# Performance work log

Measured on AMD Instinct MI355X. Metric: run time of the kernel, lower is better.

The kernel has to match this reference:

```python
import math
import jax, jax.numpy as jnp
import numpy as np


def get_alibi_slopes(n_heads: int) -> jnp.ndarray:
    def _pow2_slopes(n):
        i = jnp.arange(1, n + 1, dtype=jnp.float32)
        return jnp.power(2.0, -8.0 * i / n)
    if n_heads & (n_heads - 1) == 0:
        return _pow2_slopes(n_heads)
    nearest = 2 ** math.ceil(math.log2(n_heads))
    full = _pow2_slopes(nearest)
    half = nearest // 2
    half_slopes = _pow2_slopes(half)
    extra = full[jnp.arange(half) * 2 + 1]
    return jnp.concatenate([half_slopes, extra])[:n_heads]


def build_alibi_bias(n_heads: int, T: int, causal: bool = True) -> jnp.ndarray:
    slopes = get_alibi_slopes(n_heads)  # (H,)
    idx = jnp.arange(T)
    rel = jnp.abs(idx[:, None] - idx[None, :]).astype(jnp.float32)  # (T,T)
    bias = -slopes[:, None, None] * rel[None]  # (H,T,T)
    if causal:
        future = idx[None, :] > idx[:, None]
        bias = jnp.where(future[None], -jnp.inf, bias)
    return bias


def setup_inputs() -> dict:
    key = jax.random.key(0)
    ks = jax.random.split(key, 5)
    B, T, C = 2, 2048, 1024
    s = 0.02
    return {
        "x": jax.random.normal(ks[0], (B, T, C), dtype=jnp.float32),
        "Wq": jax.random.normal(ks[1], (C, C), dtype=jnp.float32) * s,
        "Wk": jax.random.normal(ks[2], (C, C), dtype=jnp.float32) * s,
        "Wv": jax.random.normal(ks[3], (C, C), dtype=jnp.float32) * s,
        "Wo": jax.random.normal(ks[4], (C, C), dtype=jnp.float32) * s,
    }


def reference(x, Wq, Wk, Wv, Wo):
    B, T, C = x.shape
    H = 16
    D = C // H
    scale = D ** -0.5
    # torch nn.Linear(bias=False): y = x @ W.T
    def proj_split(W):
        t = jnp.einsum('btc,dc->btd', x, W)
        return t.reshape(B, T, H, D).transpose(0, 2, 1, 3)  # (B,H,T,D)
    q, k, v = proj_split(Wq), proj_split(Wk), proj_split(Wv)
    scores = jnp.einsum('bhtd,bhsd->bhts', q, k) * scale  # (B,H,T,T)
    bias = build_alibi_bias(H, T, causal=True)  # (H,T,T)
    scores = scores + bias[None]
    attn = jax.nn.softmax(scores, axis=-1)
    out = jnp.einsum('bhts,bhsd->bhtd', attn, v)
    out = out.transpose(0, 2, 1, 3).reshape(B, T, C)
    return jnp.einsum('btc,dc->btd', out, Wo)
```

## Files before the change

### kernel.cpp

```cpp
#include <hip/hip_runtime.h>
#include <hip/hip_bf16.h>


typedef _Float16 f16;
typedef f16 f16x2 __attribute__((ext_vector_type(2)));
typedef f16 f16x4 __attribute__((ext_vector_type(4)));
typedef f16 f16x8 __attribute__((ext_vector_type(8)));
typedef float f32x4 __attribute__((ext_vector_type(4)));
typedef float f32x16 __attribute__((ext_vector_type(16)));

#define LOG2E 1.4426950408889634f
#define LDK 40
#define LDA 72
#define LDV 136

__device__ __forceinline__ f16x4 pk4(f32x4 v) {
  f16x2 a = __builtin_bit_cast(f16x2, __builtin_amdgcn_cvt_pkrtz(v[0], v[1]));
  f16x2 b = __builtin_bit_cast(f16x2, __builtin_amdgcn_cvt_pkrtz(v[2], v[3]));
  f16x4 r; r[0] = a[0]; r[1] = a[1]; r[2] = b[0]; r[3] = b[1];
  return r;
}
__device__ __forceinline__ f16x8 mkp(const float* e, int p) {
  f16x2 a = __builtin_bit_cast(f16x2, __builtin_amdgcn_cvt_pkrtz(e[4*p+0], e[4*p+1]));
  f16x2 b = __builtin_bit_cast(f16x2, __builtin_amdgcn_cvt_pkrtz(e[4*p+2], e[4*p+3]));
  f16x2 c = __builtin_bit_cast(f16x2, __builtin_amdgcn_cvt_pkrtz(e[8+4*p+0], e[8+4*p+1]));
  f16x2 d = __builtin_bit_cast(f16x2, __builtin_amdgcn_cvt_pkrtz(e[8+4*p+2], e[8+4*p+3]));
  f16x8 r;
  r[0]=a[0]; r[1]=a[1]; r[2]=b[0]; r[3]=b[1];
  r[4]=c[0]; r[5]=c[1]; r[6]=d[0]; r[7]=d[1];
  return r;
}

__global__ __launch_bounds__(256) void cvt_f32_f16(
    const float* __restrict__ x, const float* __restrict__ wq,
    const float* __restrict__ wk, const float* __restrict__ wv,
    const float* __restrict__ wo,
    f16* __restrict__ dx, f16* __restrict__ dwq, f16* __restrict__ dwk,
    f16* __restrict__ dwv, f16* __restrict__ dwo) {
  const float* src; f16* dst; int n;
  switch (blockIdx.y) {
    case 0:  src = x;  dst = dx;  n = 4194304; break;
    case 1:  src = wq; dst = dwq; n = 1048576; break;
    case 2:  src = wk; dst = dwk; n = 1048576; break;
    case 3:  src = wv; dst = dwv; n = 1048576; break;
    default: src = wo; dst = dwo; n = 1048576; break;
  }
  int i = (blockIdx.x * 256 + (int)threadIdx.x) * 8;
  if (i >= n) return;
  f32x4 a = *(const f32x4*)(src + i);
  f32x4 b = *(const f32x4*)(src + i + 4);
  f16x8 o;
  f16x4 lo4 = pk4(a), hi4 = pk4(b);
#pragma unroll
  for (int j = 0; j < 4; j++) { o[j] = lo4[j]; o[j + 4] = hi4[j]; }
  *(f16x8*)(dst + i) = o;
}

__device__ __forceinline__ void gemm_core(const f16* __restrict__ A,
                                          const f16* __restrict__ W,
                                          int m0, int n0,
                                          f16* lA, f16* lW,
                                          f32x4 acc[4][4]) {
  const int tid = threadIdx.x;
  const int lane = tid & 63, w = tid >> 6;
  const int wm = w & 1, wn = w >> 1;
  const int q = lane & 15, quad = lane >> 4;
  const int r0 = tid >> 2, c0 = (tid & 3) * 8;

  const f16* Ap = A + (m0 + r0) * 1024 + c0;
  const f16* Wp = W + (n0 + r0) * 1024 + c0;
  f16x8 a0 = *(const f16x8*)(Ap);
  f16x8 a1 = *(const f16x8*)(Ap + 64 * 1024);
  f16x8 w0 = *(const f16x8*)(Wp);
  f16x8 w1 = *(const f16x8*)(Wp + 64 * 1024);

#pragma unroll 2
  for (int r = 0; r < 32; r++) {
    const int p = r & 1;
    f16* dA = lA + p * (128 * LDK);
    f16* dW = lW + p * (128 * LDK);
    *(f16x8*)(dA + r0 * LDK + c0) = a0;
    *(f16x8*)(dA + (64 + r0) * LDK + c0) = a1;
    *(f16x8*)(dW + r0 * LDK + c0) = w0;
    *(f16x8*)(dW + (64 + r0) * LDK + c0) = w1;
    if (r + 1 < 32) {
      const int kn = (r + 1) * 32;
      a0 = *(const f16x8*)(Ap + kn);
      a1 = *(const f16x8*)(Ap + 64 * 1024 + kn);
      w0 = *(const f16x8*)(Wp + kn);
      w1 = *(const f16x8*)(Wp + 64 * 1024 + kn);
    }
    __syncthreads();
    f16x8 aF[4], bF[4];
#pragma unroll
    for (int mt = 0; mt < 4; mt++)
      aF[mt] = *(const f16x8*)(dA + (wm * 64 + mt * 16 + q) * LDK + quad * 8);
#pragma unroll
    for (int nt = 0; nt < 4; nt++)
      bF[nt] = *(const f16x8*)(dW + (wn * 64 + nt * 16 + q) * LDK + quad * 8);
#pragma unroll
    for (int mt = 0; mt < 4; mt++)
#pragma unroll
      for (int nt = 0; nt < 4; nt++)
        acc[mt][nt] = __builtin_amdgcn_mfma_f32_16x16x32_f16(aF[mt], bF[nt], acc[mt][nt], 0, 0, 0);
  }
}

__global__ __launch_bounds__(256) void qkv_proj(
    const f16* __restrict__ x16, const f16* __restrict__ wq16,
    const f16* __restrict__ wk16, const f16* __restrict__ wv16,
    f16* __restrict__ qb, f16* __restrict__ kb, f16* __restrict__ vb,
    float qscale) {
  __shared__ __align__(16) f16 lA[2 * 128 * LDK];
  __shared__ __align__(16) f16 lW[2 * 128 * LDK];
  const int m0 = blockIdx.x * 128, n0 = blockIdx.y * 128;
  const int z = blockIdx.z;
  const f16* W = (z == 0) ? wq16 : (z == 1) ? wk16 : wv16;
  f16* out = (z == 0) ? qb : (z == 1) ? kb : vb;
  const float scale = (z == 0) ? qscale : 1.0f;

  f32x4 acc[4][4];
  const f32x4 zero = {0.f, 0.f, 0.f, 0.f};
#pragma unroll
  for (int i = 0; i < 4; i++)
#pragma unroll
    for (int j = 0; j < 4; j++) acc[i][j] = zero;
  gemm_core(x16, W, m0, n0, lA, lW, acc);

  const int tid = threadIdx.x, lane = tid & 63, w = tid >> 6;
  const int wm = w & 1, wn = w >> 1, q = lane & 15, quad = lane >> 4;
#pragma unroll
  for (int mt = 0; mt < 4; mt++)
#pragma unroll
    for (int nt = 0; nt < 4; nt++) {
      int n = n0 + wn * 64 + nt * 16 + q;
      int h = n >> 6, d = n & 63;
#pragma unroll
      for (int r = 0; r < 4; r++) {
        int mm = m0 + wm * 64 + mt * 16 + quad * 4 + r;
        int bb = mm >> 11, tl = mm & 2047;
        out[((bb * 16 + h) * 2048 + tl) * 64 + d] = (f16)(acc[mt][nt][r] * scale);
      }
    }
}

__global__ __launch_bounds__(256) void attn(
    const f16* __restrict__ qB, const f16* __restrict__ kB,
    const f16* __restrict__ vB, f16* __restrict__ att) {
  __shared__ __align__(16) f16 lK[128 * LDA];
  __shared__ __align__(16) f16 lV[64 * LDV];
  const int tid = threadIdx.x, lane = tid & 63, w = tid >> 6;
  const int n5 = lane & 31, hh = lane >> 5;
  const int bh = blockIdx.x, qb_ = 15 - (int)blockIdx.y;
  const int b = bh >> 4, h = bh & 15;
  const int q0 = qb_ * 128;
  const f16* qP = qB + (bh * 2048) * 64;
  const f16* kP = kB + (bh * 2048) * 64;
  const f16* vP = vB + (bh * 2048) * 64;

  const float slope2 = __builtin_amdgcn_exp2f(-0.5f * (float)(h + 1)) * LOG2E;
  const int qg = q0 + w * 32 + n5;
  const int qlast = q0 + w * 32 + 31;
  const int wdiag = ((q0 + w * 32) >> 6) << 6;

  f16x8 qF[4];
#pragma unroll
  for (int ks = 0; ks < 4; ks++)
    qF[ks] = *(const f16x8*)(qP + qg * 64 + ks * 16 + hh * 8);

  f32x16 cinit, ot0, ot1;
#pragma unroll
  for (int i = 0; i < 16; i++) { cinit[i] = -8.0f; ot0[i] = 0.f; ot1[i] = 0.f; }
  float lsum = 0.0f;

  const int kr = tid >> 2, kc = (tid & 3) * 8;
  const int pp = kr & 31;
  const int mperm = (pp & 3) + 16 * ((pp >> 2) & 1) + 4 * ((pp >> 3) & 1) + 8 * ((pp >> 4) & 1);
  const int lkr = (kr & 32) + mperm;
  const int vp = (tid & 63) * 2, vd0 = (tid >> 6) * 8;

  f16x8 kA0, kA1, kB0, kB1, vA0, vA1, vB0, vB1;
  kA0 = *(const f16x8*)(kP + kr * 64 + kc);
  kA1 = *(const f16x8*)(kP + kr * 64 + kc + 32);
  kB0 = *(const f16x8*)(kP + (64 + kr) * 64 + kc);
  kB1 = *(const f16x8*)(kP + (64 + kr) * 64 + kc + 32);
  vA0 = *(const f16x8*)(vP + vp * 64 + vd0);
  vA1 = *(const f16x8*)(vP + (vp + 1) * 64 + vd0);
  vB0 = *(const f16x8*)(vP + vp * 64 + vd0 + 32);
  vB1 = *(const f16x8*)(vP + (vp + 1) * 64 + vd0 + 32);

  const int nstage = qb_ + 1;
  for (int stg = 0; stg < nstage; stg++) {
    const int kv0 = stg << 7;
    __syncthreads();
    *(f16x8*)(lK + lkr * LDA + kc) = kA0;
    *(f16x8*)(lK + lkr * LDA + kc + 32) = kA1;
    *(f16x8*)(lK + (64 + lkr) * LDA + kc) = kB0;
    *(f16x8*)(lK + (64 + lkr) * LDA + kc + 32) = kB1;
#pragma unroll
    for (int j = 0; j < 8; j++) {
      f16x2 t0; t0[0] = vA0[j]; t0[1] = vA1[j];
      *(f16x2*)(lV + (vd0 + j) * LDV + vp) = t0;
      f16x2 t1; t1[0] = vB0[j]; t1[1] = vB1[j];
      *(f16x2*)(lV + (vd0 + 32 + j) * LDV + vp) = t1;
    }
    __syncthreads();
    if (stg + 1 < nstage) {
      const int kn = kv0 + 128;
      kA0 = *(const f16x8*)(kP + (kn + kr) * 64 + kc);
      kA1 = *(const f16x8*)(kP + (kn + kr) * 64 + kc + 32);
      kB0 = *(const f16x8*)(kP + (kn + 64 + kr) * 64 + kc);
      kB1 = *(const f16x8*)(kP + (kn + 64 + kr) * 64 + kc + 32);
      vA0 = *(const f16x8*)(vP + (kn + vp) * 64 + vd0);
      vA1 = *(const f16x8*)(vP + (kn + vp + 1) * 64 + vd0);
      vB0 = *(const f16x8*)(vP + (kn + vp) * 64 + vd0 + 32);
      vB1 = *(const f16x8*)(vP + (kn + vp + 1) * 64 + vd0 + 32);
    }
#pragma unroll
    for (int half = 0; half < 2; half++) {
      const int kvh = kv0 + half * 64;
      if (kvh > wdiag) break;
      const bool act1 = (kvh + 32 <= qlast);
      const bool needmask = (kvh == wdiag);
      f32x16 s0 = cinit, s1 = cinit;
#pragma unroll
      for (int ks = 0; ks < 4; ks++) {
        f16x8 kf = *(const f16x8*)(lK + (half * 64 + n5) * LDA + ks * 16 + hh * 8);
        s0 = __builtin_amdgcn_mfma_f32_32x32x16_f16(kf, qF[ks], s0, 0, 0, 0);
      }
      if (act1) {
#pragma unroll
        for (int ks = 0; ks < 4; ks++) {
          f16x8 kf = *(const f16x8*)(lK + (half * 64 + 32 + n5) * LDA + ks * 16 + hh * 8);
          s1 = __builtin_amdgcn_mfma_f32_32x32x16_f16(kf, qF[ks], s1, 0, 0, 0);
        }
      }
      f16x8 pf00, pf01, pf10, pf11;
      {
        const int dQ = qg - kvh - 8 * hh;
        const float base0 = -slope2 * (float)dQ;
        float ev[16];
#pragma unroll
        for (int u = 0; u < 4; u++)
#pragma unroll
          for (int t = 0; t < 4; t++) {
            const int reg = t + 4 * u;
            const int CR = 16 * (u & 1) + 4 * (u >> 1) + t;
            float val = s0[reg] + fmaf(slope2, (float)CR, base0);
            if (needmask) val = (dQ >= CR) ? val : -1e30f;
            float e = __builtin_amdgcn_exp2f(val);
            lsum += e;
            ev[reg] = e;
          }
        pf00 = mkp(ev, 0); pf01 = mkp(ev, 1);
        if (act1) {
          const int dQ1 = dQ - 32;
          const float base1 = -slope2 * (float)dQ1;
          float ev1[16];
#pragma unroll
          for (int u = 0; u < 4; u++)
#pragma unroll
            for (int t = 0; t < 4; t++) {
              const int reg = t + 4 * u;
              const int CR = 16 * (u & 1) + 4 * (u >> 1) + t;
              float val = s1[reg] + fmaf(slope2, (float)CR, base1);
              if (needmask) val = (dQ1 >= CR) ? val : -1e30f;
              float e = __builtin_amdgcn_exp2f(val);
              lsum += e;
              ev1[reg] = e;
            }
          pf10 = mkp(ev1, 0); pf11 = mkp(ev1, 1);
        }
      }
#pragma unroll
      for (int p = 0; p < 2; p++) {
        f16x8 vf0 = *(const f16x8*)(lV + n5 * LDV + half * 64 + p * 16 + hh * 8);
        f16x8 vf1 = *(const f16x8*)(lV + (32 + n5) * LDV + half * 64 + p * 16 + hh * 8);
        f16x8 pf = p ? pf01 : pf00;
        ot0 = __builtin_amdgcn_mfma_f32_32x32x16_f16(vf0, pf, ot0, 0, 0, 0);
        ot1 = __builtin_amdgcn_mfma_f32_32x32x16_f16(vf1, pf, ot1, 0, 0, 0);
      }
      if (act1) {
#pragma unroll
        for (int p = 0; p < 2; p++) {
          f16x8 vf0 = *(const f16x8*)(lV + n5 * LDV + half * 64 + 32 + p * 16 + hh * 8);
          f16x8 vf1 = *(const f16x8*)(lV + (32 + n5) * LDV + half * 64 + 32 + p * 16 + hh * 8);
          f16x8 pf = p ? pf11 : pf10;
          ot0 = __builtin_amdgcn_mfma_f32_32x32x16_f16(vf0, pf, ot0, 0, 0, 0);
          ot1 = __builtin_amdgcn_mfma_f32_32x32x16_f16(vf1, pf, ot1, 0, 0, 0);
        }
      }
    }
  }

  lsum += __shfl_xor(lsum, 32);
  const float inv = 1.0f / lsum;

  __syncthreads();
  f16* OT = lK + w * (32 * LDA);
#pragma unroll
  for (int dt = 0; dt < 2; dt++)
#pragma unroll
    for (int u = 0; u < 4; u++) {
      f16x4 o4;
#pragma unroll
      for (int t = 0; t < 4; t++) {
        float v = (dt ? ot1[t + 4 * u] : ot0[t + 4 * u]) * inv;
        o4[t] = (f16)v;
      }
      *(f16x4*)(OT + n5 * LDA + dt * 32 + 8 * u + 4 * hh) = o4;
    }
  __syncthreads();
  const int row = lane >> 1, hr = lane & 1;
  const f16* OR = lK + w * (32 * LDA) + row * LDA + hr * 32;
  f16* dst = att + (b * 2048 + q0 + w * 32 + row) * 1024 + h * 64 + hr * 32;
#pragma unroll
  for (int j = 0; j < 4; j++)
    *(f16x8*)(dst + j * 8) = *(const f16x8*)(OR + j * 8);
}

__global__ __launch_bounds__(256) void out_proj(
    const f16* __restrict__ att, const f16* __restrict__ wo16,
    float* __restrict__ out) {
  __shared__ __align__(16) f16 lA[2 * 128 * LDK];
  __shared__ __align__(16) f16 lW[2 * 128 * LDK];
  const int m0 = blockIdx.x * 128, n0 = blockIdx.y * 128;
  f32x4 acc[4][4];
  const f32x4 zero = {0.f, 0.f, 0.f, 0.f};
#pragma unroll
  for (int i = 0; i < 4; i++)
#pragma unroll
    for (int j = 0; j < 4; j++) acc[i][j] = zero;
  gemm_core(att, wo16, m0, n0, lA, lW, acc);

  const int tid = threadIdx.x, lane = tid & 63, w = tid >> 6;
  const int wm = w & 1, wn = w >> 1, q = lane & 15, quad = lane >> 4;
#pragma unroll
  for (int mt = 0; mt < 4; mt++)
#pragma unroll
    for (int nt = 0; nt < 4; nt++) {
      int n = n0 + wn * 64 + nt * 16 + q;
#pragma unroll
      for (int r = 0; r < 4; r++) {
        int mm = m0 + wm * 64 + mt * 16 + quad * 4 + r;
        out[mm * 1024 + n] = acc[mt][nt][r];
      }
    }
}

extern "C" void kernel_launch(void* const* d_in, const int* in_sizes, int n_in,
                              void* d_out, int out_size, void* d_ws, size_t ws_size,
                              hipStream_t stream) {
  const float* x  = (const float*)d_in[0];
  const float* Wq = (const float*)d_in[1];
  const float* Wk = (const float*)d_in[2];
  const float* Wv = (const float*)d_in[3];
  const float* Wo = (const float*)d_in[4];
  char* ws = (char*)d_ws;
  const size_t MB = 1024 * 1024;
  f16* x16  = (f16*)(ws);
  f16* qb   = (f16*)(ws + 8 * MB);
  f16* kb   = (f16*)(ws + 16 * MB);
  f16* vb   = (f16*)(ws + 24 * MB);
  f16* wq16 = (f16*)(ws + 32 * MB);
  f16* wk16 = (f16*)(ws + 34 * MB);
  f16* wv16 = (f16*)(ws + 36 * MB);
  f16* wo16 = (f16*)(ws + 38 * MB);
  f16* att  = x16;

  cvt_f32_f16<<<dim3(2048, 5), 256, 0, stream>>>(x, Wq, Wk, Wv, Wo,
                                                 x16, wq16, wk16, wv16, wo16);
  qkv_proj<<<dim3(32, 8, 3), 256, 0, stream>>>(x16, wq16, wk16, wv16,
                                               qb, kb, vb, 0.125f * LOG2E);
  attn<<<dim3(32, 16), 256, 0, stream>>>(qb, kb, vb, att);
  out_proj<<<dim3(32, 8), 256, 0, stream>>>(att, wo16, (float*)d_out);
}
```

Baseline: 186.0 us.

## Split attention KV tile across two wave groups with shared-memory merge

The attention block grows to 512 threads, and two groups of 4 waves each handle one 64-key half of every 128-key stage. Previously each wave walked both halves serially. The partial output accumulators and row sums are merged through shared memory before normalisation and store. The intent is more waves in flight and shorter per-wave dependency chains. In exchange the kernel needs a reduction epilogue, extra barriers, and a larger shared buffer, and the launch bounds constrain registers.

```diff
diff --git a/kernel.cpp b/kernel.cpp
--- a/kernel.cpp
+++ b/kernel.cpp
@@ -144,12 +144,17 @@
     }
 }
 
-__global__ __launch_bounds__(256) void attn(
+__global__ __launch_bounds__(512, 4) void attn(
     const f16* __restrict__ qB, const f16* __restrict__ kB,
     const f16* __restrict__ vB, f16* __restrict__ att) {
-  __shared__ __align__(16) f16 lK[128 * LDA];
-  __shared__ __align__(16) f16 lV[64 * LDV];
+  __shared__ __align__(16) char SM[36864];
+  f16* lK = (f16*)SM;
+  f16* lV = (f16*)(SM + 18432);
+  float* mgO = (float*)SM;
+  float* mgL = (float*)(SM + 34816);
+
   const int tid = threadIdx.x, lane = tid & 63, w = tid >> 6;
+  const int wg = w & 3, grp = w >> 2;
   const int n5 = lane & 31, hh = lane >> 5;
   const int bh = blockIdx.x, qb_ = 15 - (int)blockIdx.y;
   const int b = bh >> 4, h = bh & 15;
@@ -159,9 +164,9 @@
   const f16* vP = vB + (bh * 2048) * 64;
 
   const float slope2 = __builtin_amdgcn_exp2f(-0.5f * (float)(h + 1)) * LOG2E;
-  const int qg = q0 + w * 32 + n5;
-  const int qlast = q0 + w * 32 + 31;
-  const int wdiag = ((q0 + w * 32) >> 6) << 6;
+  const int qg = q0 + wg * 32 + n5;
+  const int qlast = q0 + wg * 32 + 31;
+  const int wdiag = ((q0 + wg * 32) >> 6) << 6;
 
   f16x8 qF[4];
 #pragma unroll
@@ -173,65 +178,51 @@
   for (int i = 0; i < 16; i++) { cinit[i] = -8.0f; ot0[i] = 0.f; ot1[i] = 0.f; }
   float lsum = 0.0f;
 
-  const int kr = tid >> 2, kc = (tid & 3) * 8;
+  const int kr = tid >> 3, ks8 = (tid & 7) * 8;
   const int pp = kr & 31;
   const int mperm = (pp & 3) + 16 * ((pp >> 2) & 1) + 4 * ((pp >> 3) & 1) + 8 * ((pp >> 4) & 1);
   const int lkr = (kr & 32) + mperm;
-  const int vp = (tid & 63) * 2, vd0 = (tid >> 6) * 8;
-
-  f16x8 kA0, kA1, kB0, kB1, vA0, vA1, vB0, vB1;
-  kA0 = *(const f16x8*)(kP + kr * 64 + kc);
-  kA1 = *(const f16x8*)(kP + kr * 64 + kc + 32);
-  kB0 = *(const f16x8*)(kP + (64 + kr) * 64 + kc);
-  kB1 = *(const f16x8*)(kP + (64 + kr) * 64 + kc + 32);
-  vA0 = *(const f16x8*)(vP + vp * 64 + vd0);
-  vA1 = *(const f16x8*)(vP + (vp + 1) * 64 + vd0);
-  vB0 = *(const f16x8*)(vP + vp * 64 + vd0 + 32);
-  vB1 = *(const f16x8*)(vP + (vp + 1) * 64 + vd0 + 32);
+  const int vp = (tid & 63) * 2, vd = (tid >> 6) * 8;
+
+  f16x8 kA, kB_, vA, vB_;
+  kA  = *(const f16x8*)(kP + kr * 64 + ks8);
+  kB_ = *(const f16x8*)(kP + (64 + kr) * 64 + ks8);
+  vA  = *(const f16x8*)(vP + vp * 64 + vd);
+  vB_ = *(const f16x8*)(vP + (vp + 1) * 64 + vd);
 
   const int nstage = qb_ + 1;
   for (int stg = 0; stg < nstage; stg++) {
     const int kv0 = stg << 7;
     __syncthreads();
-    *(f16x8*)(lK + lkr * LDA + kc) = kA0;
-    *(f16x8*)(lK + lkr * LDA + kc + 32) = kA1;
-    *(f16x8*)(lK + (64 + lkr) * LDA + kc) = kB0;
-    *(f16x8*)(lK + (64 + lkr) * LDA + kc + 32) = kB1;
+    *(f16x8*)(lK + lkr * LDA + ks8) = kA;
+    *(f16x8*)(lK + (64 + lkr) * LDA + ks8) = kB_;
 #pragma unroll
     for (int j = 0; j < 8; j++) {
-      f16x2 t0; t0[0] = vA0[j]; t0[1] = vA1[j];
-      *(f16x2*)(lV + (vd0 + j) * LDV + vp) = t0;
-      f16x2 t1; t1[0] = vB0[j]; t1[1] = vB1[j];
-      *(f16x2*)(lV + (vd0 + 32 + j) * LDV + vp) = t1;
+      f16x2 t; t[0] = vA[j]; t[1] = vB_[j];
+      *(f16x2*)(lV + (vd + j) * LDV + vp) = t;
     }
     __syncthreads();
     if (stg + 1 < nstage) {
       const int kn = kv0 + 128;
-      kA0 = *(const f16x8*)(kP + (kn + kr) * 64 + kc);
-      kA1 = *(const f16x8*)(kP + (kn + kr) * 64 + kc + 32);
-      kB0 = *(const f16x8*)(kP + (kn + 64 + kr) * 64 + kc);
-      kB1 = *(const f16x8*)(kP + (kn + 64 + kr) * 64 + kc + 32);
-      vA0 = *(const f16x8*)(vP + (kn + vp) * 64 + vd0);
-      vA1 = *(const f16x8*)(vP + (kn + vp + 1) * 64 + vd0);
-      vB0 = *(const f16x8*)(vP + (kn + vp) * 64 + vd0 + 32);
-      vB1 = *(const f16x8*)(vP + (kn + vp + 1) * 64 + vd0 + 32);
-    }
-#pragma unroll
-    for (int half = 0; half < 2; half++) {
-      const int kvh = kv0 + half * 64;
-      if (kvh > wdiag) break;
+      kA  = *(const f16x8*)(kP + (kn + kr) * 64 + ks8);
+      kB_ = *(const f16x8*)(kP + (kn + 64 + kr) * 64 + ks8);
+      vA  = *(const f16x8*)(vP + (kn + vp) * 64 + vd);
+      vB_ = *(const f16x8*)(vP + (kn + vp + 1) * 64 + vd);
+    }
+    const int kvh = kv0 + grp * 64;
+    if (kvh <= wdiag) {
       const bool act1 = (kvh + 32 <= qlast);
       const bool needmask = (kvh == wdiag);
       f32x16 s0 = cinit, s1 = cinit;
 #pragma unroll
       for (int ks = 0; ks < 4; ks++) {
-        f16x8 kf = *(const f16x8*)(lK + (half * 64 + n5) * LDA + ks * 16 + hh * 8);
+        f16x8 kf = *(const f16x8*)(lK + (grp * 64 + n5) * LDA + ks * 16 + hh * 8);
         s0 = __builtin_amdgcn_mfma_f32_32x32x16_f16(kf, qF[ks], s0, 0, 0, 0);
       }
       if (act1) {
 #pragma unroll
         for (int ks = 0; ks < 4; ks++) {
-          f16x8 kf = *(const f16x8*)(lK + (half * 64 + 32 + n5) * LDA + ks * 16 + hh * 8);
+          f16x8 kf = *(const f16x8*)(lK + (grp * 64 + 32 + n5) * LDA + ks * 16 + hh * 8);
           s1 = __builtin_amdgcn_mfma_f32_32x32x16_f16(kf, qF[ks], s1, 0, 0, 0);
         }
       }
@@ -274,8 +265,8 @@
       }
 #pragma unroll
       for (int p = 0; p < 2; p++) {
-        f16x8 vf0 = *(const f16x8*)(lV + n5 * LDV + half * 64 + p * 16 + hh * 8);
-        f16x8 vf1 = *(const f16x8*)(lV + (32 + n5) * LDV + half * 64 + p * 16 + hh * 8);
+        f16x8 vf0 = *(const f16x8*)(lV + n5 * LDV + grp * 64 + p * 16 + hh * 8);
+        f16x8 vf1 = *(const f16x8*)(lV + (32 + n5) * LDV + grp * 64 + p * 16 + hh * 8);
         f16x8 pf = p ? pf01 : pf00;
         ot0 = __builtin_amdgcn_mfma_f32_32x32x16_f16(vf0, pf, ot0, 0, 0, 0);
         ot1 = __builtin_amdgcn_mfma_f32_32x32x16_f16(vf1, pf, ot1, 0, 0, 0);
@@ -283,8 +274,8 @@
       if (act1) {
 #pragma unroll
         for (int p = 0; p < 2; p++) {
-          f16x8 vf0 = *(const f16x8*)(lV + n5 * LDV + half * 64 + 32 + p * 16 + hh * 8);
-          f16x8 vf1 = *(const f16x8*)(lV + (32 + n5) * LDV + half * 64 + 32 + p * 16 + hh * 8);
+          f16x8 vf0 = *(const f16x8*)(lV + n5 * LDV + grp * 64 + 32 + p * 16 + hh * 8);
+          f16x8 vf1 = *(const f16x8*)(lV + (32 + n5) * LDV + grp * 64 + 32 + p * 16 + hh * 8);
           f16x8 pf = p ? pf11 : pf10;
           ot0 = __builtin_amdgcn_mfma_f32_32x32x16_f16(vf0, pf, ot0, 0, 0, 0);
           ot1 = __builtin_amdgcn_mfma_f32_32x32x16_f16(vf1, pf, ot1, 0, 0, 0);
@@ -294,29 +285,61 @@
   }
 
   lsum += __shfl_xor(lsum, 32);
-  const float inv = 1.0f / lsum;
-
   __syncthreads();
-  f16* OT = lK + w * (32 * LDA);
-#pragma unroll
-  for (int dt = 0; dt < 2; dt++)
-#pragma unroll
-    for (int u = 0; u < 4; u++) {
-      f16x4 o4;
-#pragma unroll
-      for (int t = 0; t < 4; t++) {
-        float v = (dt ? ot1[t + 4 * u] : ot0[t + 4 * u]) * inv;
-        o4[t] = (f16)v;
-      }
-      *(f16x4*)(OT + n5 * LDA + dt * 32 + 8 * u + 4 * hh) = o4;
-    }
+  if (grp == 1) {
+#pragma unroll
+    for (int dt = 0; dt < 2; dt++)
+#pragma unroll
+      for (int u = 0; u < 4; u++) {
+        f32x4 v4;
+#pragma unroll
+        for (int t = 0; t < 4; t++) v4[t] = (dt ? ot1[t + 4 * u] : ot0[t + 4 * u]);
+        *(f32x4*)(mgO + (wg * 32 + n5) * 68 + dt * 32 + 8 * u + 4 * hh) = v4;
+      }
+    mgL[wg * 64 + lane] = lsum;
+  }
   __syncthreads();
-  const int row = lane >> 1, hr = lane & 1;
-  const f16* OR = lK + w * (32 * LDA) + row * LDA + hr * 32;
-  f16* dst = att + (b * 2048 + q0 + w * 32 + row) * 1024 + h * 64 + hr * 32;
-#pragma unroll
-  for (int j = 0; j < 4; j++)
-    *(f16x8*)(dst + j * 8) = *(const f16x8*)(OR + j * 8);
+  float inv = 0.0f;
+  if (grp == 0) {
+    lsum += mgL[wg * 64 + lane];
+    inv = 1.0f / lsum;
+#pragma unroll
+    for (int dt = 0; dt < 2; dt++)
+#pragma unroll
+      for (int u = 0; u < 4; u++) {
+        f32x4 v4 = *(const f32x4*)(mgO + (wg * 32 + n5) * 68 + dt * 32 + 8 * u + 4 * hh);
+#pragma unroll
+        for (int t = 0; t < 4; t++) {
+          if (dt) ot1[t + 4 * u] += v4[t];
+          else    ot0[t + 4 * u] += v4[t];
+        }
+      }
+  }
+  __syncthreads();
+  if (grp == 0) {
+    f16* OT = lK + wg * (32 * LDA);
+#pragma unroll
+    for (int dt = 0; dt < 2; dt++)
+#pragma unroll
+      for (int u = 0; u < 4; u++) {
+        f16x4 o4;
+#pragma unroll
+        for (int t = 0; t < 4; t++) {
+          float v = (dt ? ot1[t + 4 * u] : ot0[t + 4 * u]) * inv;
+          o4[t] = (f16)v;
+        }
+        *(f16x4*)(OT + n5 * LDA + dt * 32 + 8 * u + 4 * hh) = o4;
+      }
+  }
+  __syncthreads();
+  if (grp == 0) {
+    const int row = lane >> 1, hr = lane & 1;
+    const f16* OR = lK + wg * (32 * LDA) + row * LDA + hr * 32;
+    f16* dst = att + (b * 2048 + q0 + wg * 32 + row) * 1024 + h * 64 + hr * 32;
+#pragma unroll
+    for (int j = 0; j < 4; j++)
+      *(f16x8*)(dst + j * 8) = *(const f16x8*)(OR + j * 8);
+  }
 }
 
 __global__ __launch_bounds__(256) void out_proj(
@@ -372,6 +395,6 @@
                                                  x16, wq16, wk16, wv16, wo16);
   qkv_proj<<<dim3(32, 8, 3), 256, 0, stream>>>(x16, wq16, wk16, wv16,
                                                qb, kb, vb, 0.125f * LOG2E);
-  attn<<<dim3(32, 16), 256, 0, stream>>>(qb, kb, vb, att);
+  attn<<<dim3(32, 16), 512, 0, stream>>>(qb, kb, vb, att);
   out_proj<<<dim3(32, 8), 256, 0, stream>>>(att, wo16, (float*)d_out);
 }
```

New measurement: 214.2 us. +15.2%, slower.
